# Optimization experiments

Measured on AMD Instinct MI355X. Metric: run time of the kernel, lower is better.

The kernel has to match this reference:

```python
import jax, jax.numpy as jnp
from jax import lax
import numpy as np

V, D_MODEL, N_LAYER, D_STATE, D_CONV, EXPAND = 32000, 1024, 2, 16, 4, 2
D_INNER = EXPAND * D_MODEL          # 2048
DT_RANK = D_MODEL // 16             # 64 (ceil(d_model/16) in mamba_ssm)
B, L = 2, 2048


def setup_inputs() -> dict:
    key = jax.random.key(0)
    ks = jax.random.split(key, 10)
    f = lambda k, shape, s=0.02: (jax.random.normal(k, shape) * s).astype(jnp.float32)
    return {
        "tokens": jax.random.randint(ks[0], (B, L), 0, V),
        "embedding": f(ks[1], (V, D_MODEL)),
        "in_proj_w": f(ks[2], (N_LAYER, 2 * D_INNER, D_MODEL)),
        "conv_w": f(ks[3], (N_LAYER, D_INNER, D_CONV), 0.2),
        "conv_b": jnp.zeros((N_LAYER, D_INNER), jnp.float32),
        "x_proj_w": f(ks[4], (N_LAYER, DT_RANK + 2 * D_STATE, D_INNER)),
        "dt_proj_w": f(ks[5], (N_LAYER, D_INNER, DT_RANK), 0.1),
        "dt_proj_b": f(ks[6], (N_LAYER, D_INNER), 0.5),
        # S4D-real init: A_log = log(1..d_state), A = -exp(A_log)
        "A_log": jnp.tile(jnp.log(jnp.arange(1, D_STATE + 1, dtype=jnp.float32))[None, None, :], (N_LAYER, D_INNER, 1)),
        "D_skip": jnp.ones((N_LAYER, D_INNER), jnp.float32),
        "out_proj_w": f(ks[7], (N_LAYER, D_MODEL, D_INNER)),
        "norm_gamma": jnp.ones((D_MODEL,), jnp.float32),
        "norm_beta": jnp.zeros((D_MODEL,), jnp.float32),
        "lm_head_w": f(ks[8], (V, D_MODEL)),
    }


def _causal_dw_conv(x, w, b):
    # x: [B,L,C], w: [C,K] depthwise causal conv (kernel K=4)
    K = w.shape[1]
    xp = jnp.pad(x, ((0, 0), (K - 1, 0), (0, 0)))
    y = sum(xp[:, k:k + x.shape[1], :] * w[:, k] for k in range(K))
    return y + b


def _mamba_block(x, in_w, cw, cb, xp_w, dt_w, dt_b, A_log, D_skip, out_w):
    # in_proj -> split into u (ssm branch) and z (gate)
    xz = jnp.einsum('bld,ed->ble', x, in_w)          # [B,L,2*d_inner]
    u, z = jnp.split(xz, 2, axis=-1)
    u = jax.nn.silu(_causal_dw_conv(u, cw, cb))      # [B,L,d_inner]
    x_dbl = jnp.einsum('ble,re->blr', u, xp_w)       # [B,L,dt_rank+2*d_state]
    dt, B_ssm, C_ssm = jnp.split(x_dbl, [DT_RANK, DT_RANK + D_STATE], axis=-1)
    delta = jax.nn.softplus(jnp.einsum('blr,er->ble', dt, dt_w) + dt_b)  # [B,L,d_inner]
    A = -jnp.exp(A_log)                              # [d_inner,d_state]

    def step(h, inp):
        u_t, d_t, b_t, c_t = inp                     # [B,e],[B,e],[B,s],[B,s]
        h = h * jnp.exp(d_t[:, :, None] * A) + (d_t * u_t)[:, :, None] * b_t[:, None, :]
        y = jnp.einsum('bes,bs->be', h, c_t)
        return h, y

    h0 = jnp.zeros((u.shape[0], D_INNER, D_STATE), u.dtype)
    _, ys = lax.scan(step, h0, (u.swapaxes(0, 1), delta.swapaxes(0, 1),
                                B_ssm.swapaxes(0, 1), C_ssm.swapaxes(0, 1)))
    y = ys.swapaxes(0, 1) + u * D_skip               # D skip connection
    y = y * jax.nn.silu(z)                           # gating
    return jnp.einsum('ble,de->bld', y, out_w)


def reference(tokens, embedding, in_proj_w, conv_w, conv_b, x_proj_w, dt_proj_w,
              dt_proj_b, A_log, D_skip, out_proj_w, norm_gamma, norm_beta, lm_head_w):
    x = embedding[tokens]                            # [B,L,d_model]
    for i in range(N_LAYER):
        x = _mamba_block(x, in_proj_w[i], conv_w[i], conv_b[i], x_proj_w[i],
                         dt_proj_w[i], dt_proj_b[i], A_log[i], D_skip[i], out_proj_w[i])
    mu = jnp.mean(x, axis=-1, keepdims=True)
    var = jnp.mean(jnp.square(x - mu), axis=-1, keepdims=True)
    xn = (x - mu) * lax.rsqrt(var + 1e-5) * norm_gamma + norm_beta
    return jnp.einsum('bld,vd->blv', xn, lm_head_w)  # logits [B,L,V]
```

## Files before the change

kernel.cpp:

```cpp
#include <hip/hip_runtime.h>
#include <hip/hip_bf16.h>

#define L_SEQ 2048
#define BATCH 2
#define DM    1024
#define DI    2048
#define DS    16
#define DTR   64
#define DBLC  96
#define VOCAB 32000
#define BL    (BATCH * L_SEQ)
#define NCH   32
#define CHL   (L_SEQ / NCH)
#define EL    8

typedef unsigned short u16;
typedef short s8v  __attribute__((ext_vector_type(8)));
typedef float f32x4 __attribute__((ext_vector_type(4)));

typedef __attribute__((address_space(1))) const void* as1cv;
typedef __attribute__((address_space(3))) void*       as3v;

static __device__ __forceinline__ u16 f2bf(float f) {
    unsigned u = __builtin_bit_cast(unsigned, f);
    u += 0x7fffu + ((u >> 16) & 1u);
    return (u16)(u >> 16);
}

__global__ __launch_bounds__(256) void cvt_bf16_kernel(
    const float* __restrict__ in, u16* __restrict__ out, int n8)
{
    int i = blockIdx.x * 256 + threadIdx.x;
    if (i >= n8) return;
    const float4* p = (const float4*)in + 2 * (size_t)i;
    float4 a = p[0], b = p[1];
    s8v o;
    o[0] = (short)f2bf(a.x); o[1] = (short)f2bf(a.y);
    o[2] = (short)f2bf(a.z); o[3] = (short)f2bf(a.w);
    o[4] = (short)f2bf(b.x); o[5] = (short)f2bf(b.y);
    o[6] = (short)f2bf(b.z); o[7] = (short)f2bf(b.w);
    ((s8v*)out)[i] = o;
}

__global__ __launch_bounds__(256) void cvt2_bf16_kernel(
    const float* __restrict__ inA, u16* __restrict__ outA, int n8A,
    const float* __restrict__ inB, u16* __restrict__ outB, int n8B)
{
    int i = blockIdx.x * 256 + threadIdx.x;
    const float* src; u16* dst; int idx;
    if (i < n8A) { src = inA; dst = outA; idx = i; }
    else if (i < n8A + n8B) { src = inB; dst = outB; idx = i - n8A; }
    else return;
    const float4* p = (const float4*)src + 2 * (size_t)idx;
    float4 a = p[0], b = p[1];
    s8v o;
    o[0] = (short)f2bf(a.x); o[1] = (short)f2bf(a.y);
    o[2] = (short)f2bf(a.z); o[3] = (short)f2bf(a.w);
    o[4] = (short)f2bf(b.x); o[5] = (short)f2bf(b.y);
    o[6] = (short)f2bf(b.z); o[7] = (short)f2bf(b.w);
    ((s8v*)dst)[idx] = o;
}

__global__ __launch_bounds__(256) void embed_kernel(
    const int* __restrict__ tok, const float* __restrict__ emb,
    u16* __restrict__ Xb)
{
    int row = blockIdx.x;
    int t = tok[row];
    float4 v = ((const float4*)(emb + (size_t)t * DM))[threadIdx.x];
    ushort4 o;
    o.x = f2bf(v.x); o.y = f2bf(v.y); o.z = f2bf(v.z); o.w = f2bf(v.w);
    ((ushort4*)(Xb + (size_t)row * DM))[threadIdx.x] = o;
}

template<int MODE>
__global__ __launch_bounds__(512) void gemm_deep(
    const u16* __restrict__ A, int lda,
    const u16* __restrict__ Bt, int ldb,
    float* __restrict__ C0, float* __restrict__ C1,
    int ldc0, int K)
{
    __shared__ __align__(16) u16 As[4][256 * 32];
    __shared__ __align__(16) u16 Bs[4][256 * 32];

    const int tid  = threadIdx.x;
    const int lane = tid & 63;
    const int wv   = tid >> 6;
    const int bm = blockIdx.x * 256;
    const int bn = blockIdx.y * 256;

    const int ks = (lane & 3) ^ ((lane >> 3) & 3);
    const int lr = lane >> 2;
    const u16* ag0 = A  + (size_t)(bm + wv * 32 + lr) * lda + ks * 8;
    const u16* ag1 = ag0 + 16 * (size_t)lda;
    const u16* bg0 = Bt + (size_t)(bn + wv * 32 + lr) * ldb + ks * 8;
    const u16* bg1 = bg0 + 16 * (size_t)ldb;
    const int lo0 = wv * 1024;
    const int lo1 = wv * 1024 + 512;

    const int li = lane & 15;
    const int kc = lane >> 4;
    const int wr = (wv >> 2) * 128;
    const int wc = (wv & 3) * 64;
    const int fo = (kc ^ ((li >> 1) & 3)) * 8;

    f32x4 acc[8][4];
#pragma unroll
    for (int m = 0; m < 8; ++m)
#pragma unroll
        for (int n = 0; n < 4; ++n) acc[m][n] = (f32x4)0.f;

#define STG(buf, kk)                                                           \
    do {                                                                       \
        __builtin_amdgcn_global_load_lds((as1cv)(ag0 + (kk)),                  \
            (as3v)&As[buf][lo0], 16, 0, 0);                                    \
        __builtin_amdgcn_global_load_lds((as1cv)(ag1 + (kk)),                  \
            (as3v)&As[buf][lo1], 16, 0, 0);                                    \
        __builtin_amdgcn_global_load_lds((as1cv)(bg0 + (kk)),                  \
            (as3v)&Bs[buf][lo0], 16, 0, 0);                                    \
        __builtin_amdgcn_global_load_lds((as1cv)(bg1 + (kk)),                  \
            (as3v)&Bs[buf][lo1], 16, 0, 0);                                    \
    } while (0)

    const int nt = K >> 5;
    STG(0, 0);
    STG(1, 32);
    STG(2, 64);
    asm volatile("s_waitcnt vmcnt(8)" ::: "memory");
    __builtin_amdgcn_s_barrier();
    __builtin_amdgcn_sched_barrier(0);

    for (int t = 0; t < nt; ++t) {
        if (t + 3 < nt) STG((t + 3) & 3, (t + 3) << 5);

        const u16* Ab = &As[t & 3][0];
        const u16* Bb = &Bs[t & 3][0];
        s8v af[8], bf[4];
#pragma unroll
        for (int m = 0; m < 8; ++m)
            af[m] = *(const s8v*)&Ab[(wr + m * 16 + li) * 32 + fo];
#pragma unroll
        for (int n = 0; n < 4; ++n)
            bf[n] = *(const s8v*)&Bb[(wc + n * 16 + li) * 32 + fo];

        __builtin_amdgcn_s_setprio(1);
#pragma unroll
        for (int m = 0; m < 4; ++m)
#pragma unroll
            for (int n = 0; n < 4; ++n)
                acc[m][n] = __builtin_amdgcn_mfma_f32_16x16x32_bf16(
                    af[m], bf[n], acc[m][n], 0, 0, 0);
        __builtin_amdgcn_s_setprio(0);
        __builtin_amdgcn_s_setprio(1);
#pragma unroll
        for (int m = 4; m < 8; ++m)
#pragma unroll
            for (int n = 0; n < 4; ++n)
                acc[m][n] = __builtin_amdgcn_mfma_f32_16x16x32_bf16(
                    af[m], bf[n], acc[m][n], 0, 0, 0);
        __builtin_amdgcn_s_setprio(0);

        if (t + 1 < nt) {
            if (t + 3 < nt)
                asm volatile("s_waitcnt vmcnt(8)" ::: "memory");
            else if (t + 2 < nt)
                asm volatile("s_waitcnt vmcnt(4)" ::: "memory");
            else
                asm volatile("s_waitcnt vmcnt(0)" ::: "memory");
            __builtin_amdgcn_s_barrier();
            __builtin_amdgcn_sched_barrier(0);
        }
    }
#undef STG

#pragma unroll
    for (int m = 0; m < 8; ++m) {
#pragma unroll
        for (int j = 0; j < 4; ++j) {
            int row = bm + wr + m * 16 + kc * 4 + j;
#pragma unroll
            for (int n = 0; n < 4; ++n) {
                int col = bn + wc + n * 16 + li;
                float v = acc[m][n][j];
                if (MODE == 0) {
                    C0[(size_t)row * ldc0 + col] = v;
                } else {
                    if (bn < DI) C0[(size_t)row * DI + col] = v;
                    else         C1[(size_t)row * DI + col - DI] = v;
                }
            }
        }
    }
}

__global__ __launch_bounds__(256) void gemm_bb2(
    const u16* __restrict__ A, int lda,
    const u16* __restrict__ Bt, int ldb,
    float* __restrict__ C0, u16* __restrict__ Cb, int ldc0, int K)
{
    __shared__ __align__(16) u16 As[2][128 * 32];
    __shared__ __align__(16) u16 Bs[2][128 * 32];

    const int tid  = threadIdx.x;
    const int lane = tid & 63;
    const int wv   = tid >> 6;
    const int bm = blockIdx.x * 128;
    const int bn = blockIdx.y * 128;

    const int ks = (lane & 3) ^ ((lane >> 3) & 3);
    const int sr = wv * 32 + (lane >> 2);
    const u16* ag0 = A  + (size_t)(bm + sr) * lda + ks * 8;
    const u16* ag1 = ag0 + 16 * (size_t)lda;
    const u16* bg0 = Bt + (size_t)(bn + sr) * ldb + ks * 8;
    const u16* bg1 = bg0 + 16 * (size_t)ldb;
    const int lo0 = wv * 1024;
    const int lo1 = wv * 1024 + 512;

    const int li = lane & 15;
    const int kc = lane >> 4;
    const int wr = (wv >> 1) * 64;
    const int wc = (wv & 1) * 64;
    const int fo = (kc ^ ((li >> 1) & 3)) * 8;

    f32x4 acc[4][4];
#pragma unroll
    for (int m = 0; m < 4; ++m)
#pragma unroll
        for (int n = 0; n < 4; ++n) acc[m][n] = (f32x4)0.f;

#define STAGE(buf, kk)                                                         \
    do {                                                                       \
        __builtin_amdgcn_global_load_lds((as1cv)(ag0 + (kk)),                  \
            (as3v)&As[buf][lo0], 16, 0, 0);                                    \
        __builtin_amdgcn_global_load_lds((as1cv)(ag1 + (kk)),                  \
            (as3v)&As[buf][lo1], 16, 0, 0);                                    \
        __builtin_amdgcn_global_load_lds((as1cv)(bg0 + (kk)),                  \
            (as3v)&Bs[buf][lo0], 16, 0, 0);                                    \
        __builtin_amdgcn_global_load_lds((as1cv)(bg1 + (kk)),                  \
            (as3v)&Bs[buf][lo1], 16, 0, 0);                                    \
    } while (0)

    const int nt = K >> 5;
    STAGE(0, 0);
    asm volatile("s_waitcnt vmcnt(0)" ::: "memory");
    __builtin_amdgcn_s_barrier();
    __builtin_amdgcn_sched_barrier(0);

    int cur = 0;
    for (int t = 0; t < nt; ++t) {
        if (t + 1 < nt) STAGE(cur ^ 1, (t + 1) << 5);

        const u16* Ab = &As[cur][0];
        const u16* Bb = &Bs[cur][0];
        s8v af[4], bf[4];
#pragma unroll
        for (int m = 0; m < 4; ++m)
            af[m] = *(const s8v*)&Ab[(wr + m * 16 + li) * 32 + fo];
#pragma unroll
        for (int n = 0; n < 4; ++n)
            bf[n] = *(const s8v*)&Bb[(wc + n * 16 + li) * 32 + fo];
#pragma unroll
        for (int m = 0; m < 4; ++m)
#pragma unroll
            for (int n = 0; n < 4; ++n)
                acc[m][n] = __builtin_amdgcn_mfma_f32_16x16x32_bf16(
                    af[m], bf[n], acc[m][n], 0, 0, 0);

        if (t + 1 < nt) {
            asm volatile("s_waitcnt vmcnt(0)" ::: "memory");
            __builtin_amdgcn_s_barrier();
            __builtin_amdgcn_sched_barrier(0);
            cur ^= 1;
        }
    }
#undef STAGE

#pragma unroll
    for (int m = 0; m < 4; ++m) {
#pragma unroll
        for (int j = 0; j < 4; ++j) {
            int row = bm + wr + m * 16 + kc * 4 + j;
#pragma unroll
            for (int n = 0; n < 4; ++n) {
                int col = bn + wc + n * 16 + li;
                float v = acc[m][n][j];
                C0[(size_t)row * ldc0 + col] = v;
                Cb[(size_t)row * ldc0 + col] = f2bf(v);
            }
        }
    }
}

template<int EPI, bool NGUARD, bool SPLITK>
__global__ __launch_bounds__(256) void sgemm_bt(
    const float* __restrict__ A, int lda,
    const float* __restrict__ Bt, int ldb,
    float* __restrict__ C, int ldc,
    const float* __restrict__ bias,
    int M, int N, int K, int kchunk)
{
    __shared__ float As[16][132];
    __shared__ float Bs[16][132];

    const int tid = threadIdx.x;
    const int bm = blockIdx.y * 128;
    const int bn = blockIdx.x * 128;

    int k0 = 0, kend = K;
    if (SPLITK) {
        k0 = blockIdx.z * kchunk;
        kend = k0 + kchunk; if (kend > K) kend = K;
        C += (size_t)blockIdx.z * (size_t)M * (size_t)ldc;
    }

    const int tx = tid & 15;
    const int ty = tid >> 4;
    const int lr = tid >> 2;
    const int lc = (tid & 3) << 2;

    float acc[8][8];
#pragma unroll
    for (int i = 0; i < 8; ++i)
#pragma unroll
        for (int j = 0; j < 8; ++j) acc[i][j] = 0.f;

    for (int kk = k0; kk < kend; kk += 16) {
#pragma unroll
        for (int p = 0; p < 2; ++p) {
            int r = lr + p * 64;
            float4 v = *(const float4*)(A + (size_t)(bm + r) * lda + kk + lc);
            As[lc + 0][r] = v.x; As[lc + 1][r] = v.y;
            As[lc + 2][r] = v.z; As[lc + 3][r] = v.w;
        }
#pragma unroll
        for (int p = 0; p < 2; ++p) {
            int r = lr + p * 64;
            float4 v = make_float4(0.f, 0.f, 0.f, 0.f);
            if (!NGUARD || (bn + r) < N)
                v = *(const float4*)(Bt + (size_t)(bn + r) * ldb + kk + lc);
            Bs[lc + 0][r] = v.x; Bs[lc + 1][r] = v.y;
            Bs[lc + 2][r] = v.z; Bs[lc + 3][r] = v.w;
        }
        __syncthreads();
#pragma unroll
        for (int k = 0; k < 16; ++k) {
            float4 a0 = *(const float4*)&As[k][ty * 4];
            float4 a1 = *(const float4*)&As[k][64 + ty * 4];
            float4 b0 = *(const float4*)&Bs[k][tx * 4];
            float4 b1 = *(const float4*)&Bs[k][64 + tx * 4];
            float av[8] = {a0.x, a0.y, a0.z, a0.w, a1.x, a1.y, a1.z, a1.w};
            float bv[8] = {b0.x, b0.y, b0.z, b0.w, b1.x, b1.y, b1.z, b1.w};
#pragma unroll
            for (int i = 0; i < 8; ++i)
#pragma unroll
                for (int j = 0; j < 8; ++j)
                    acc[i][j] += av[i] * bv[j];
        }
        __syncthreads();
    }

#pragma unroll
    for (int p = 0; p < 2; ++p) {
#pragma unroll
        for (int ii = 0; ii < 4; ++ii) {
            int row = bm + p * 64 + ty * 4 + ii;
#pragma unroll
            for (int q = 0; q < 2; ++q) {
                int col = bn + q * 64 + tx * 4;
                if (NGUARD && col >= N) continue;
                float4 v;
                float* vp = &v.x;
#pragma unroll
                for (int jj = 0; jj < 4; ++jj) {
                    float x = acc[p * 4 + ii][q * 4 + jj];
                    if (EPI == 1) {
                        x += bias[col + jj];
                        x = (x > 20.f) ? x : log1pf(__expf(x));
                    }
                    vp[jj] = x;
                }
                *(float4*)(C + (size_t)row * ldc + col) = v;
            }
        }
    }
}

__global__ __launch_bounds__(256) void reduce8_kernel(
    const float* __restrict__ part, float* __restrict__ out, int n)
{
    int i = blockIdx.x * 256 + threadIdx.x;
    if (i < n) {
        float s = 0.f;
#pragma unroll
        for (int j = 0; j < 8; ++j) s += part[(size_t)j * n + i];
        out[i] = s;
    }
}

__global__ __launch_bounds__(256) void conv_silu_kernel(
    const float* __restrict__ XZu, const float* __restrict__ cw,
    const float* __restrict__ cb, float* __restrict__ U)
{
    int idx = blockIdx.x * 256 + threadIdx.x;
    int c4 = idx & 511;
    int row = idx >> 9;
    int t = row & (L_SEQ - 1);
    int c = c4 << 2;

    float4 acc;
    acc.x = cb[c]; acc.y = cb[c + 1]; acc.z = cb[c + 2]; acc.w = cb[c + 3];
    float4 w0 = *(const float4*)(cw + (size_t)(c + 0) * 4);
    float4 w1 = *(const float4*)(cw + (size_t)(c + 1) * 4);
    float4 w2 = *(const float4*)(cw + (size_t)(c + 2) * 4);
    float4 w3 = *(const float4*)(cw + (size_t)(c + 3) * 4);
#pragma unroll
    for (int k = 0; k < 4; ++k) {
        int tt = t - 3 + k;
        if (tt >= 0) {
            float4 xv = *(const float4*)(XZu + (size_t)(row - 3 + k) * DI + c);
            acc.x += xv.x * ((&w0.x)[k]);
            acc.y += xv.y * ((&w1.x)[k]);
            acc.z += xv.z * ((&w2.x)[k]);
            acc.w += xv.w * ((&w3.x)[k]);
        }
    }
    acc.x = acc.x / (1.f + __expf(-acc.x));
    acc.y = acc.y / (1.f + __expf(-acc.y));
    acc.z = acc.z / (1.f + __expf(-acc.z));
    acc.w = acc.w / (1.f + __expf(-acc.w));
    *(float4*)(U + (size_t)row * DI + c) = acc;
}

__global__ __launch_bounds__(256) void scan_fused(
    const float* __restrict__ U, const float* __restrict__ DELTA,
    const float* __restrict__ DBL, const float* __restrict__ ZF,
    const float* __restrict__ A_log, const float* __restrict__ Dskip,
    u16* __restrict__ Yb)
{
    __shared__ float ps[EL][NCH][DS][2];
    __shared__ float hs[EL][NCH][DS];

    const int tid   = threadIdx.x;
    const int el    = tid & (EL - 1);
    const int chunk = tid >> 3;
    const int bid   = blockIdx.x;
    const int b     = bid >> 8;
    const int e     = (bid & 255) * EL + el;
    const int t0    = chunk * CHL;

    float Ae[DS];
#pragma unroll
    for (int s = 0; s < DS; ++s)
        Ae[s] = -__expf(A_log[(size_t)e * DS + s]);

    const float* up = U     + (size_t)b * L_SEQ * DI + e;
    const float* dp = DELTA + (size_t)b * L_SEQ * DI + e;
    const float* zp = ZF    + (size_t)b * L_SEQ * DI + e;
    const float* bp = DBL   + ((size_t)b * L_SEQ + t0) * DBLC + DTR;
    const float* cp = bp + DS;
    u16* yp = Yb + (size_t)b * L_SEQ * DI + e;

    float P[DS], S[DS];
#pragma unroll
    for (int s = 0; s < DS; ++s) { P[s] = 1.f; S[s] = 0.f; }

    {
        float u0 = up[(size_t)t0 * DI];
        float d0 = dp[(size_t)t0 * DI];
        float4 B0[4];
#pragma unroll
        for (int q = 0; q < 4; ++q) B0[q] = *(const float4*)(bp + q * 4);

        for (int i = 0; i < CHL; ++i) {
            float u1 = 0.f, d1 = 0.f;
            float4 B1[4] = {};
            if (i + 1 < CHL) {
                u1 = up[(size_t)(t0 + i + 1) * DI];
                d1 = dp[(size_t)(t0 + i + 1) * DI];
#pragma unroll
                for (int q = 0; q < 4; ++q)
                    B1[q] = *(const float4*)(bp + (i + 1) * DBLC + q * 4);
            }
            float du = d0 * u0;
            const float* Bf = (const float*)&B0[0];
#pragma unroll
            for (int s = 0; s < DS; ++s) {
                float a = __expf(d0 * Ae[s]);
                P[s] *= a;
                S[s] = S[s] * a + du * Bf[s];
            }
            u0 = u1; d0 = d1;
#pragma unroll
            for (int q = 0; q < 4; ++q) B0[q] = B1[q];
        }
    }
#pragma unroll
    for (int s = 0; s < DS; ++s) {
        ps[el][chunk][s][0] = P[s];
        ps[el][chunk][s][1] = S[s];
    }
    __syncthreads();

    if (tid < EL * DS) {
        int pel = tid >> 4;
        int s   = tid & 15;
        float h = 0.f;
#pragma unroll
        for (int c = 0; c < NCH; ++c) {
            hs[pel][c][s] = h;
            h = ps[pel][c][s][0] * h + ps[pel][c][s][1];
        }
    }
    __syncthreads();

    float Dk = Dskip[e];
    float h[DS];
#pragma unroll
    for (int s = 0; s < DS; ++s) h[s] = hs[el][chunk][s];

    {
        float u0 = up[(size_t)t0 * DI];
        float d0 = dp[(size_t)t0 * DI];
        float z0 = zp[(size_t)t0 * DI];
        float4 B0[4], C0[4];
#pragma unroll
        for (int q = 0; q < 4; ++q) {
            B0[q] = *(const float4*)(bp + q * 4);
            C0[q] = *(const float4*)(cp + q * 4);
        }

        for (int i = 0; i < CHL; ++i) {
            float u1 = 0.f, d1 = 0.f, z1 = 0.f;
            float4 B1[4] = {}, C1[4] = {};
            if (i + 1 < CHL) {
                u1 = up[(size_t)(t0 + i + 1) * DI];
                d1 = dp[(size_t)(t0 + i + 1) * DI];
                z1 = zp[(size_t)(t0 + i + 1) * DI];
#pragma unroll
                for (int q = 0; q < 4; ++q) {
                    B1[q] = *(const float4*)(bp + (i + 1) * DBLC + q * 4);
                    C1[q] = *(const float4*)(cp + (i + 1) * DBLC + q * 4);
                }
            }
            float du = d0 * u0;
            const float* Bf = (const float*)&B0[0];
            const float* Cf = (const float*)&C0[0];
            float y0 = 0.f, y1 = 0.f, y2 = 0.f, y3 = 0.f;
#pragma unroll
            for (int s = 0; s < DS; ++s) {
                float a = __expf(d0 * Ae[s]);
                h[s] = h[s] * a + du * Bf[s];
                float hc = h[s] * Cf[s];
                if ((s & 3) == 0) y0 += hc;
                else if ((s & 3) == 1) y1 += hc;
                else if ((s & 3) == 2) y2 += hc;
                else y3 += hc;
            }
            float p = (y0 + y1) + (y2 + y3);
            float g = z0 / (1.f + __expf(-z0));
            yp[(size_t)(t0 + i) * DI] = f2bf((p + u0 * Dk) * g);
            u0 = u1; d0 = d1; z0 = z1;
#pragma unroll
            for (int q = 0; q < 4; ++q) { B0[q] = B1[q]; C0[q] = C1[q]; }
        }
    }
}

__global__ __launch_bounds__(256) void layernorm_kernel(
    const float* __restrict__ X, const float* __restrict__ g,
    const float* __restrict__ be, u16* __restrict__ XNb)
{
    __shared__ float red[4];
    int row = blockIdx.x;
    int tid = threadIdx.x;
    float4 v = ((const float4*)(X + (size_t)row * DM))[tid];

    float ssum = v.x + v.y + v.z + v.w;
#pragma unroll
    for (int o = 32; o >= 1; o >>= 1) ssum += __shfl_xor(ssum, o);
    if ((tid & 63) == 0) red[tid >> 6] = ssum;
    __syncthreads();
    float mean = (red[0] + red[1] + red[2] + red[3]) * (1.f / DM);
    __syncthreads();

    float dx = v.x - mean, dy = v.y - mean, dz = v.z - mean, dw = v.w - mean;
    float sq = dx * dx + dy * dy + dz * dz + dw * dw;
#pragma unroll
    for (int o = 32; o >= 1; o >>= 1) sq += __shfl_xor(sq, o);
    if ((tid & 63) == 0) red[tid >> 6] = sq;
    __syncthreads();
    float var = (red[0] + red[1] + red[2] + red[3]) * (1.f / DM);
    float rs = rsqrtf(var + 1e-5f);

    float4 gv = ((const float4*)g)[tid];
    float4 bv = ((const float4*)be)[tid];
    ushort4 o;
    o.x = f2bf(dx * rs * gv.x + bv.x);
    o.y = f2bf(dy * rs * gv.y + bv.y);
    o.z = f2bf(dz * rs * gv.z + bv.z);
    o.w = f2bf(dw * rs * gv.w + bv.w);
    ((ushort4*)(XNb + (size_t)row * DM))[tid] = o;
}

extern "C" void kernel_launch(void* const* d_in, const int* in_sizes, int n_in,
                              void* d_out, int out_size, void* d_ws, size_t ws_size,
                              hipStream_t stream)
{
    const int*   tokens = (const int*)d_in[0];
    const float* emb    = (const float*)d_in[1];
    const float* in_w   = (const float*)d_in[2];
    const float* conv_w = (const float*)d_in[3];
    const float* conv_b = (const float*)d_in[4];
    const float* xp_w   = (const float*)d_in[5];
    const float* dt_w   = (const float*)d_in[6];
    const float* dt_b   = (const float*)d_in[7];
    const float* A_log  = (const float*)d_in[8];
    const float* Dskip  = (const float*)d_in[9];
    const float* out_w  = (const float*)d_in[10];
    const float* gamma  = (const float*)d_in[11];
    const float* beta   = (const float*)d_in[12];
    const float* lm_w   = (const float*)d_in[13];
    float* out = (float*)d_out;

    float* ws = (float*)d_ws;
    size_t off = 0;
    float* X     = ws + off; off += (size_t)BL * DM;
    float* XZu   = ws + off; off += (size_t)BL * DI;
    float* U     = ws + off; off += (size_t)BL * DI;
    float* ZF    = ws + off; off += (size_t)BL * DI;
    float* DELTA = ws + off; off += (size_t)BL * DI;
    float* DBL   = ws + off; off += (size_t)BL * DBLC;
    u16* Xb     = (u16*)(ws + off); off += (size_t)BL * DM / 2;
    u16* wb_in  = (u16*)(ws + off); off += (size_t)2 * DI * DM / 2;
    u16* wb_out = (u16*)(ws + off); off += (size_t)DM * DI / 2;
    u16* Yb    = (u16*)XZu;
    u16* wb_lm = (u16*)XZu;
    float* PART = DELTA;
    u16* XNb   = Xb;

    embed_kernel<<<BL, 256, 0, stream>>>(tokens, emb, Xb);

    const int SCAN_GRID = BATCH * (DI / EL);

    for (int l = 0; l < 2; ++l) {
        const float* cwp = conv_w + (size_t)l * DI * 4;
        const float* cbp = conv_b + (size_t)l * DI;
        const float* xw  = xp_w   + (size_t)l * DBLC * DI;
        const float* dw  = dt_w   + (size_t)l * DI * DTR;
        const float* dbp = dt_b   + (size_t)l * DI;
        const float* alp = A_log  + (size_t)l * DI * DS;
        const float* dkp = Dskip  + (size_t)l * DI;

        const int n8i = 2 * DI * DM / 8, n8o = DM * DI / 8;
        cvt2_bf16_kernel<<<(n8i + n8o + 255) / 256, 256, 0, stream>>>(
            in_w + (size_t)l * 2 * DI * DM, wb_in, n8i,
            out_w + (size_t)l * DM * DI, wb_out, n8o);

        gemm_deep<1><<<dim3(16, 16), 512, 0, stream>>>(
            Xb, DM, wb_in, DM, XZu, ZF, 0, DM);
        conv_silu_kernel<<<(BL * DI / 4) / 256, 256, 0, stream>>>(XZu, cwp, cbp, U);
        sgemm_bt<0, true, true><<<dim3(1, 32, 8), 256, 0, stream>>>(
            U, DI, xw, DI, PART, DBLC, nullptr, BL, DBLC, DI, DI / 8);
        reduce8_kernel<<<(BL * DBLC + 255) / 256, 256, 0, stream>>>(
            PART, DBL, BL * DBLC);
        sgemm_bt<1, false, false><<<dim3(16, 32), 256, 0, stream>>>(
            DBL, DBLC, dw, DTR, DELTA, DI, dbp, BL, DI, DTR, 0);
        scan_fused<<<SCAN_GRID, 256, 0, stream>>>(
            U, DELTA, DBL, ZF, alp, dkp, Yb);
        gemm_bb2<<<dim3(32, 8), 256, 0, stream>>>(
            Yb, DI, wb_out, DI, X, Xb, DM, DI);
    }

    cvt_bf16_kernel<<<((size_t)VOCAB * DM / 8 + 255) / 256, 256, 0, stream>>>(
        lm_w, wb_lm, VOCAB * DM / 8);

    layernorm_kernel<<<BL, 256, 0, stream>>>(X, gamma, beta, XNb);

    gemm_deep<0><<<dim3(16, 125), 512, 0, stream>>>(
        XNb, DM, wb_lm, DM, out, nullptr, VOCAB, DM);
}
```

Before: 1.107 ms.

## Restructure bf16 GEMM main loop into 8-phase interleaved load/MFMA schedule

Result: faster. 1.004 ms, median of 3 (-9.2%).

```diff
diff --git a/kernel.cpp b/kernel.cpp
--- a/kernel.cpp
+++ b/kernel.cpp
@@ -74,7 +74,7 @@
 }
 
 template<int MODE>
-__global__ __launch_bounds__(512) void gemm_deep(
+__global__ __launch_bounds__(512) void gemm_8p(
     const u16* __restrict__ A, int lda,
     const u16* __restrict__ Bt, int ldb,
     float* __restrict__ C0, float* __restrict__ C1,
@@ -91,12 +91,11 @@
 
     const int ks = (lane & 3) ^ ((lane >> 3) & 3);
     const int lr = lane >> 2;
-    const u16* ag0 = A  + (size_t)(bm + wv * 32 + lr) * lda + ks * 8;
-    const u16* ag1 = ag0 + 16 * (size_t)lda;
-    const u16* bg0 = Bt + (size_t)(bn + wv * 32 + lr) * ldb + ks * 8;
-    const u16* bg1 = bg0 + 16 * (size_t)ldb;
-    const int lo0 = wv * 1024;
-    const int lo1 = wv * 1024 + 512;
+    const u16* ag = A  + (size_t)(bm + wv * 16 + lr) * lda + ks * 8;
+    const u16* bg = Bt + (size_t)(bn + wv * 16 + lr) * ldb + ks * 8;
+    const size_t a128 = (size_t)128 * lda;
+    const size_t b128 = (size_t)128 * ldb;
+    const int lo = wv * 16 * 32;
 
     const int li = lane & 15;
     const int kc = lane >> 4;
@@ -110,68 +109,100 @@
 #pragma unroll
         for (int n = 0; n < 4; ++n) acc[m][n] = (f32x4)0.f;
 
-#define STG(buf, kk)                                                           \
+#define STA8(reg, koff)                                                        \
     do {                                                                       \
-        __builtin_amdgcn_global_load_lds((as1cv)(ag0 + (kk)),                  \
-            (as3v)&As[buf][lo0], 16, 0, 0);                                    \
-        __builtin_amdgcn_global_load_lds((as1cv)(ag1 + (kk)),                  \
-            (as3v)&As[buf][lo1], 16, 0, 0);                                    \
-        __builtin_amdgcn_global_load_lds((as1cv)(bg0 + (kk)),                  \
-            (as3v)&Bs[buf][lo0], 16, 0, 0);                                    \
-        __builtin_amdgcn_global_load_lds((as1cv)(bg1 + (kk)),                  \
-            (as3v)&Bs[buf][lo1], 16, 0, 0);                                    \
+        __builtin_amdgcn_global_load_lds((as1cv)(ag + (koff)),                 \
+            (as3v)&As[reg][lo], 16, 0, 0);                                     \
+        __builtin_amdgcn_global_load_lds((as1cv)(ag + a128 + (koff)),          \
+            (as3v)&As[reg][lo + 128 * 32], 16, 0, 0);                          \
     } while (0)
-
-    const int nt = K >> 5;
-    STG(0, 0);
-    STG(1, 32);
-    STG(2, 64);
-    asm volatile("s_waitcnt vmcnt(8)" ::: "memory");
-    __builtin_amdgcn_s_barrier();
+#define STB8(reg, koff)                                                        \
+    do {                                                                       \
+        __builtin_amdgcn_global_load_lds((as1cv)(bg + (koff)),                 \
+            (as3v)&Bs[reg][lo], 16, 0, 0);                                     \
+        __builtin_amdgcn_global_load_lds((as1cv)(bg + b128 + (koff)),          \
+            (as3v)&Bs[reg][lo + 128 * 32], 16, 0, 0);                          \
+    } while (0)
+#define MFMA16(n0i, n1i)                                                       \
+    do {                                                                       \
+        __builtin_amdgcn_s_setprio(1);                                         \
+        _Pragma("unroll")                                                      \
+        for (int m = 0; m < 8; ++m) {                                          \
+            acc[m][n0i] = __builtin_amdgcn_mfma_f32_16x16x32_bf16(             \
+                af[m], b0, acc[m][n0i], 0, 0, 0);                              \
+            acc[m][n1i] = __builtin_amdgcn_mfma_f32_16x16x32_bf16(             \
+                af[m], b1, acc[m][n1i], 0, 0, 0);                              \
+        }                                                                      \
+        __builtin_amdgcn_s_setprio(0);                                         \
+    } while (0)
+#define BAR()  __builtin_amdgcn_s_barrier()
+#define LGKM() do { asm volatile("s_waitcnt lgkmcnt(0)" ::: "memory");         \
+                    __builtin_amdgcn_sched_barrier(0); } while (0)
+
+    const int nt = K >> 6;
+    STA8(0, 0); STB8(0, 0);
+    STA8(1, 32); STB8(1, 32);
+    asm volatile("s_waitcnt vmcnt(4)" ::: "memory");
+    BAR();
     __builtin_amdgcn_sched_barrier(0);
 
     for (int t = 0; t < nt; ++t) {
-        if (t + 3 < nt) STG((t + 3) & 3, (t + 3) << 5);
-
-        const u16* Ab = &As[t & 3][0];
-        const u16* Bb = &Bs[t & 3][0];
-        s8v af[8], bf[4];
+        const int d = (t & 1) * 2;
+        const int e = d ^ 2;
+        const int ko = (t + 1) << 6;
+        const bool st = (t + 1 < nt);
+        const u16* A0 = &As[d][0];
+        const u16* A1 = &As[d + 1][0];
+        const u16* B0 = &Bs[d][0];
+        const u16* B1 = &Bs[d + 1][0];
+        s8v af[8], b0, b1;
+
 #pragma unroll
         for (int m = 0; m < 8; ++m)
-            af[m] = *(const s8v*)&Ab[(wr + m * 16 + li) * 32 + fo];
-#pragma unroll
-        for (int n = 0; n < 4; ++n)
-            bf[n] = *(const s8v*)&Bb[(wc + n * 16 + li) * 32 + fo];
-
-        __builtin_amdgcn_s_setprio(1);
-#pragma unroll
-        for (int m = 0; m < 4; ++m)
-#pragma unroll
-            for (int n = 0; n < 4; ++n)
-                acc[m][n] = __builtin_amdgcn_mfma_f32_16x16x32_bf16(
-                    af[m], bf[n], acc[m][n], 0, 0, 0);
-        __builtin_amdgcn_s_setprio(0);
-        __builtin_amdgcn_s_setprio(1);
-#pragma unroll
-        for (int m = 4; m < 8; ++m)
-#pragma unroll
-            for (int n = 0; n < 4; ++n)
-                acc[m][n] = __builtin_amdgcn_mfma_f32_16x16x32_bf16(
-                    af[m], bf[n], acc[m][n], 0, 0, 0);
-        __builtin_amdgcn_s_setprio(0);
-
-        if (t + 1 < nt) {
-            if (t + 3 < nt)
-                asm volatile("s_waitcnt vmcnt(8)" ::: "memory");
-            else if (t + 2 < nt)
-                asm volatile("s_waitcnt vmcnt(4)" ::: "memory");
-            else
-                asm volatile("s_waitcnt vmcnt(0)" ::: "memory");
-            __builtin_amdgcn_s_barrier();
+            af[m] = *(const s8v*)&A0[(wr + m * 16 + li) * 32 + fo];
+        b0 = *(const s8v*)&B0[(wc + li) * 32 + fo];
+        b1 = *(const s8v*)&B0[(wc + 16 + li) * 32 + fo];
+        if (st) STA8(e, ko);
+        BAR(); LGKM();
+        MFMA16(0, 1);
+        BAR();
+
+        b0 = *(const s8v*)&B0[(wc + 32 + li) * 32 + fo];
+        b1 = *(const s8v*)&B0[(wc + 48 + li) * 32 + fo];
+        if (st) STB8(e, ko);
+        BAR(); LGKM();
+        MFMA16(2, 3);
+        if (st) asm volatile("s_waitcnt vmcnt(4)" ::: "memory");
+        else    asm volatile("s_waitcnt vmcnt(0)" ::: "memory");
+        BAR();
+        __builtin_amdgcn_sched_barrier(0);
+
+#pragma unroll
+        for (int m = 0; m < 8; ++m)
+            af[m] = *(const s8v*)&A1[(wr + m * 16 + li) * 32 + fo];
+        b0 = *(const s8v*)&B1[(wc + li) * 32 + fo];
+        b1 = *(const s8v*)&B1[(wc + 16 + li) * 32 + fo];
+        if (st) STA8(e + 1, ko + 32);
+        BAR(); LGKM();
+        MFMA16(0, 1);
+        BAR();
+
+        b0 = *(const s8v*)&B1[(wc + 32 + li) * 32 + fo];
+        b1 = *(const s8v*)&B1[(wc + 48 + li) * 32 + fo];
+        if (st) STB8(e + 1, ko + 32);
+        BAR(); LGKM();
+        MFMA16(2, 3);
+        if (st) {
+            asm volatile("s_waitcnt vmcnt(4)" ::: "memory");
+            BAR();
             __builtin_amdgcn_sched_barrier(0);
         }
     }
-#undef STG
+#undef STA8
+#undef STB8
+#undef MFMA16
+#undef BAR
+#undef LGKM
 
 #pragma unroll
     for (int m = 0; m < 8; ++m) {
@@ -656,7 +687,7 @@
             in_w + (size_t)l * 2 * DI * DM, wb_in, n8i,
             out_w + (size_t)l * DM * DI, wb_out, n8o);
 
-        gemm_deep<1><<<dim3(16, 16), 512, 0, stream>>>(
+        gemm_8p<1><<<dim3(16, 16), 512, 0, stream>>>(
             Xb, DM, wb_in, DM, XZu, ZF, 0, DM);
         conv_silu_kernel<<<(BL * DI / 4) / 256, 256, 0, stream>>>(XZu, cwp, cbp, U);
         sgemm_bt<0, true, true><<<dim3(1, 32, 8), 256, 0, stream>>>(
@@ -676,6 +707,6 @@
 
     layernorm_kernel<<<BL, 256, 0, stream>>>(X, gamma, beta, XNb);
 
-    gemm_deep<0><<<dim3(16, 125), 512, 0, stream>>>(
+    gemm_8p<0><<<dim3(16, 125), 512, 0, stream>>>(
         XNb, DM, wb_lm, DM, out, nullptr, VOCAB, DM);
 }
```
